# Kernel optimization log

Hardware: AMD Instinct MI355X
Metric: run time of the kernel (lower is better)

## Reference

```python
import jax, jax.numpy as jnp
import numpy as np
import math


def _strided_value_mask(L, S, dtype):
    # mask_line[L + d] == 0 when |d| is a power-of-two stride in {2,4,...,<=L};
    # value_mask[i, j] = mask_line[L - i + j], i.e. zero where |j - i| is such a stride.
    diff = jnp.abs(jnp.arange(L)[:, None] - jnp.arange(S)[None, :])  # [L, S]
    vm = jnp.ones((L, S), dtype=dtype)
    stride = 2
    while stride <= L:
        vm = vm * (diff != stride).astype(dtype)
        stride *= 2
    return vm


def setup_inputs() -> dict:
    key = jax.random.key(0)
    k1, k2, k3 = jax.random.split(key, 3)
    B, L, H, E = 4, 2048, 8, 64
    D = 64
    return {
        "queries": jax.random.normal(k1, (B, L, H, E), dtype=jnp.float32),
        "keys": jax.random.normal(k2, (B, L, H, E), dtype=jnp.float32),
        "values": jax.random.normal(k3, (B, L, H, D), dtype=jnp.float32),
    }


def reference(queries, keys, values):
    B, L, H, E = queries.shape
    S = keys.shape[1]
    scale = 1.0 / math.sqrt(E)

    # raw scores [B, H, L, S]
    scores = jnp.einsum("blhe,bshe->bhls", queries, keys)
    # multiplicative strided mask (zeroes scores at power-of-two offsets)
    vm = _strided_value_mask(L, S, scores.dtype)  # [L, S]
    scores = scores * vm
    # causal mask: upper triangle -> -inf (mask_flag=True, attn_mask=None path)
    causal = jnp.triu(jnp.ones((L, S), dtype=bool), k=1)
    scores = jnp.where(causal, -jnp.inf, scores)

    # dropout p=0.0 (eval) -> identity
    A = jax.nn.softmax(scale * scores, axis=-1)
    V = jnp.einsum("bhls,bshd->blhd", A, values)
    return V
```

## Files before the change

kernel.cpp:

```cpp
#include <hip/hip_runtime.h>
#include <hip/hip_bf16.h>
#include <stdint.h>

typedef __attribute__((ext_vector_type(8))) short short8;
typedef __attribute__((ext_vector_type(16))) float f32x16;

namespace {
constexpr int NB = 4, NL = 2048, NH = 8, NE = 64, ND = 64;
constexpr float KS = 0.125f * 1.44269504f;
constexpr int NCHUNK = 40;
constexpr int RECSZ  = 8320;
constexpr int KSTEP  = 64 * NH * NE;
}

__device__ const unsigned char TG[40] = {
  3,7,7,10,11,11,11,14,14,15,15,15,15,
  6,6,9,9,10,10,12,12,13,13,13,13,14,14,
  2,5,5,8,8,8,9,12,12,
  4,4,1,0};
__device__ const unsigned char TT0[40] = {
  0,0,16,0,0,16,32,0,16,0,16,32,48,
  0,14,0,14,16,30,0,14,0,14,28,42,32,46,
  0,0,12,0,12,24,28,28,40,
  0,10,0,0};
__device__ const unsigned char TT1[40] = {
  16,16,32,16,16,32,48,16,32,16,32,48,64,
  14,28,14,28,30,44,14,28,14,28,42,56,46,60,
  12,12,24,12,24,36,40,40,52,
  10,20,8,4};
__device__ const unsigned char TREC[40] = {
  3,10,11,18,21,22,23,32,33,36,37,38,39,
  8,9,15,16,19,20,24,25,28,29,30,31,34,35,
  2,6,7,12,13,14,17,26,27,
  4,5,1,0};
__device__ const unsigned char CUMD[16] = {0,1,2,3,4,6,8,10,12,15,18,21,24,28,32,36};
__device__ const unsigned char NCHD[16] = {1,1,1,1,2,2,2,2,3,3,3,3,4,4,4,4};

__device__ __forceinline__ ushort bfb(float x) {
  __hip_bfloat16 b(x);
  return __builtin_bit_cast(ushort, b);
}
__device__ __forceinline__ uint32_t pkbf(float lo, float hi) {
  return (uint32_t)bfb(lo) | ((uint32_t)bfb(hi) << 16);
}
__device__ __forceinline__ void glds16(const void* g, void* l) {
  __builtin_amdgcn_global_load_lds(
      (const __attribute__((address_space(1))) void*)g,
      (__attribute__((address_space(3))) void*)l, 16, 0, 0);
}

#define COMPUTE(TT, SUB, KB, VB) do {                                       \
    const int kv0_ = (TT) * 32;                                             \
    f32x16 s;                                                               \
    _Pragma("unroll")                                                       \
    for (int i_ = 0; i_ < 16; ++i_) s[i_] = 0.f;                            \
    { const char* kb_ = (const char*)(KB) + ((SUB)*32 + ln31) * 128;        \
      _Pragma("unroll")                                                     \
      for (int st_ = 0; st_ < 4; ++st_) {                                   \
        short8 kf_ = *(const short8*)(kb_ + ((st_*32 + hi*16) ^ rsw));      \
        s = __builtin_amdgcn_mfma_f32_32x32x16_bf16(kf_, qf[st_], s, 0,0,0);\
      } }                                                                   \
    const int delta_ = q0w - kv0_;                                          \
    const int qrelh_ = (qi - kv0_) - 4 * hi;                                \
    if ((TT) == tw) {                          \
      _Pragma("unroll")                                                     \
      for (int r_ = 0; r_ < 16; ++r_) {                                     \
        const int cr_ = (r_ & 3) + 8 * (r_ >> 2);                           \
        int diff_ = qrelh_ - cr_;                                           \
        float lg_ = s[r_];                                                  \
        bool p2_ = (diff_ > 1) & ((diff_ & (diff_ - 1)) == 0);              \
        lg_ = p2_ ? 0.f : lg_;                                              \
        lg_ = (diff_ < 0) ? -__builtin_inff() : lg_;                        \
        s[r_] = exp2f(lg_);                                                 \
      }                                                                     \
    } else {                                                                \
      int pmax_ = 1 << (31 - __clz(delta_ + 31));                           \
      if (pmax_ >= delta_ - 31) {        \
        _Pragma("unroll")                                                   \
        for (int r_ = 0; r_ < 16; ++r_) {                                   \
          const int cr_ = (r_ & 3) + 8 * (r_ >> 2);                         \
          int diff_ = qrelh_ - cr_;                                         \
          bool p2_ = (diff_ > 1) & ((diff_ & (diff_ - 1)) == 0);            \
          s[r_] = exp2f(p2_ ? 0.f : s[r_]);                                 \
        }                                                                   \
      } else {                                        \
        _Pragma("unroll")                                                   \
        for (int r_ = 0; r_ < 16; ++r_) s[r_] = exp2f(s[r_]);               \
      }                                                                     \
    }                                                                       \
    uint32_t w0_ = pkbf(s[0],  s[1]),  w1_ = pkbf(s[2],  s[3]);             \
    uint32_t w2_ = pkbf(s[4],  s[5]),  w3_ = pkbf(s[6],  s[7]);             \
    uint32_t w4_ = pkbf(s[8],  s[9]),  w5_ = pkbf(s[10], s[11]);            \
    uint32_t w6_ = pkbf(s[12], s[13]), w7_ = pkbf(s[14], s[15]);            \
    uint32_t y0_ = __shfl_xor(hi ? w0_ : w2_, 32);                          \
    uint32_t y1_ = __shfl_xor(hi ? w1_ : w3_, 32);                          \
    uint32_t y2_ = __shfl_xor(hi ? w4_ : w6_, 32);                          \
    uint32_t y3_ = __shfl_xor(hi ? w5_ : w7_, 32);                          \
    union { short8 v; uint32_t u[4]; } f0_, f1_;                            \
    if (hi == 0) {                                                          \
      f0_.u[0] = w0_; f0_.u[1] = w1_; f0_.u[2] = y0_; f0_.u[3] = y1_;       \
      f1_.u[0] = w4_; f1_.u[1] = w5_; f1_.u[2] = y2_; f1_.u[3] = y3_;       \
    } else {                                                                \
      f0_.u[0] = y0_; f0_.u[1] = y1_; f0_.u[2] = w2_; f0_.u[3] = w3_;       \
      f1_.u[0] = y2_; f1_.u[1] = y3_; f1_.u[2] = w6_; f1_.u[3] = w7_;       \
    }                                                                       \
    { const char* vr0_ = (const char*)(VB) + ln31 * 128;                    \
      const char* vr1_ = (const char*)(VB) + (32 + ln31) * 128;             \
      short8 a00_ = *(const short8*)(vr0_ + (((SUB)*64      + hi*16) ^ rsw));\
      short8 a01_ = *(const short8*)(vr0_ + (((SUB)*64 + 32 + hi*16) ^ rsw));\
      short8 a10_ = *(const short8*)(vr1_ + (((SUB)*64      + hi*16) ^ rsw));\
      short8 a11_ = *(const short8*)(vr1_ + (((SUB)*64 + 32 + hi*16) ^ rsw));\
      acc0 = __builtin_amdgcn_mfma_f32_32x32x16_bf16(a00_, f0_.v, acc0, 0,0,0); \
      acc0 = __builtin_amdgcn_mfma_f32_32x32x16_bf16(a01_, f1_.v, acc0, 0,0,0); \
      acc1 = __builtin_amdgcn_mfma_f32_32x32x16_bf16(a10_, f0_.v, acc1, 0,0,0); \
      acc1 = __builtin_amdgcn_mfma_f32_32x32x16_bf16(a11_, f1_.v, acc1, 0,0,0); \
      accl = __builtin_amdgcn_mfma_f32_32x32x16_bf16(onesv, f0_.v, accl, 0,0,0);\
      accl = __builtin_amdgcn_mfma_f32_32x32x16_bf16(onesv, f1_.v, accl, 0,0,0);\
    }                                                                       \
  } while (0)

#define LD(RR) do {                                                         \
    const float* kp_ = kpp + (size_t)(RR) * KSTEP;                          \
    const float* vp_ = vpp + (size_t)(RR) * KSTEP;                          \
    kx0 = *(const float4*)(kp_);      kx1 = *(const float4*)(kp_ + 4);      \
    kx2 = *(const float4*)(kp_ + 8);  kx3 = *(const float4*)(kp_ + 12);     \
    vx0 = *(const float4*)(vp_);               vx1 = *(const float4*)(vp_ + NH*ND); \
    vx2 = *(const float4*)(vp_ + 2*NH*ND);     vx3 = *(const float4*)(vp_ + 3*NH*ND); \
  } while (0)

#define STG(KB, VB) do {                                                    \
    uint4 kwA = { pkbf(kx0.x,kx0.y), pkbf(kx0.z,kx0.w),                     \
                  pkbf(kx1.x,kx1.y), pkbf(kx1.z,kx1.w) };                   \
    uint4 kwB = { pkbf(kx2.x,kx2.y), pkbf(kx2.z,kx2.w),                     \
                  pkbf(kx3.x,kx3.y), pkbf(kx3.z,kx3.w) };                   \
    *(uint4*)((KB) + krow*128 + ( kcol2        ^ kswz)) = kwA;              \
    *(uint4*)((KB) + krow*128 + ((kcol2 + 16)  ^ kswz)) = kwB;              \
    _Pragma("unroll")                                                       \
    for (int j_ = 0; j_ < 4; ++j_) {                                        \
      int d_ = vd0 + j_;                                                    \
      char* vr_ = (VB) + d_*128;                                            \
      int vs_ = (d_ & 7) << 4;                                              \
      *(uint32_t*)(vr_ + ((vk0*2    ) ^ vs_)) = pkbf(vx0[j_], vx1[j_]);     \
      *(uint32_t*)(vr_ + ((vk0*2 + 4) ^ vs_)) = pkbf(vx2[j_], vx3[j_]);     \
    }                                                                       \
  } while (0)

__global__ __launch_bounds__(256)
void convkv(const float* __restrict__ Kg, const float* __restrict__ Vg,
            char* __restrict__ kimg, char* __restrict__ vimg)
{
  const int id = blockIdx.x;
  const int kr = id & 31, bh = id >> 5;
  const int b = bh >> 3, h = bh & 7;
  const int tid = threadIdx.x;

  __shared__ float vt[64 * 64];

  const int key_in = tid >> 2;
  const int e0     = (tid & 3) * 16;
  {
    const float* vp = Vg + (((size_t)b * NL + kr * 64 + key_in) * NH + h) * ND + e0;
    float* dst = vt + key_in * 64 + e0;
    *(float4*)(dst)      = *(const float4*)(vp);
    *(float4*)(dst + 4)  = *(const float4*)(vp + 4);
    *(float4*)(dst + 8)  = *(const float4*)(vp + 8);
    *(float4*)(dst + 12) = *(const float4*)(vp + 12);
  }
  {
    const float* kp = Kg + (((size_t)b * NL + kr * 64 + key_in) * NH + h) * NE + e0;
    float4 a = *(const float4*)kp,     c = *(const float4*)(kp + 4);
    float4 d2 = *(const float4*)(kp + 8), f = *(const float4*)(kp + 12);
    uint4 wA = { pkbf(a.x,a.y), pkbf(a.z,a.w), pkbf(c.x,c.y), pkbf(c.z,c.w) };
    uint4 wB = { pkbf(d2.x,d2.y), pkbf(d2.z,d2.w), pkbf(f.x,f.y), pkbf(f.z,f.w) };
    char* ko = kimg + ((size_t)bh * 32 + kr) * 8192 + key_in * 128;
    const int C = (key_in & 7) << 4;
    *(uint4*)(ko + ((2 * e0)      ^ C)) = wA;
    *(uint4*)(ko + ((2 * e0 + 16) ^ C)) = wB;
  }
  __syncthreads();
  char* vo0 = vimg + ((size_t)bh * 32 + kr) * 8192;
  #pragma unroll
  for (int it = 0; it < 2; ++it) {
    int lin = it * 256 + tid;
    int d = lin & 63, kg = lin >> 6;
    const float* col = vt + kg * 8 * 64 + d;
    uint4 w = { pkbf(col[0], col[64]),   pkbf(col[128], col[192]),
                pkbf(col[256], col[320]), pkbf(col[384], col[448]) };
    *(uint4*)(vo0 + d * 128 + ((kg * 16) ^ ((d & 7) << 4))) = w;
  }
}

__global__ __launch_bounds__(256, 4)
void sattn_dma(const float* __restrict__ Qg, const char* __restrict__ kimg,
               const char* __restrict__ vimg, float* __restrict__ W)
{
  const int id = blockIdx.x;
  const int bh = id & 31;
  const int e  = id >> 5;
  const int g  = TG[e];
  const int t0 = TT0[e], t1 = TT1[e];
  float* rec = W + (size_t)(bh * NCHUNK + TREC[e]) * RECSZ;
  const int b = bh >> 3, h = bh & 7;

  const int tid  = threadIdx.x;
  const int wave = tid >> 6;
  const int lane = tid & 63;
  const int ln31 = lane & 31;
  const int hi   = lane >> 5;

  __shared__ __align__(16) char smem[2 * 16384];

  const int q0w = g * 128 + wave * 32;
  const int qi  = q0w + ln31;
  const int tw  = 4 * g + wave;
  const int rsw = (ln31 & 7) << 4;

  const char* kb_img = kimg + ((size_t)bh * 32 + (t0 >> 1)) * 8192;
  const char* vb_img = vimg + ((size_t)bh * 32 + (t0 >> 1)) * 8192;

#define STAGE(RR, PP) do {                                                  \
    const char* gb_ = (wave < 2 ? kb_img : vb_img)                          \
                      + (size_t)(RR) * 8192 + (wave & 1) * 4096;            \
    char* lb_ = smem + (PP) * 16384 + (wave < 2 ? 0 : 8192)                 \
                + (wave & 1) * 4096;                                        \
    _Pragma("unroll")                                                       \
    for (int c_ = 0; c_ < 4; ++c_)                                          \
      glds16(gb_ + c_ * 1024 + lane * 16, lb_ + c_ * 1024);                 \
  } while (0)

  short8 qf[4];
  {
    const float* qp = Qg + (((size_t)b * NL + qi) * NH + h) * NE;
    #pragma unroll
    for (int st = 0; st < 4; ++st) {
      const float* qpe = qp + st * 16 + hi * 8;
      union { short8 v; uint32_t u[4]; } f;
      #pragma unroll
      for (int j = 0; j < 4; ++j)
        f.u[j] = pkbf(qpe[2 * j] * KS, qpe[2 * j + 1] * KS);
      qf[st] = f.v;
    }
  }
  short8 onesv;
  {
    union { short8 v; uint32_t u[4]; } o;
    #pragma unroll
    for (int j = 0; j < 4; ++j) o.u[j] = 0x3F803F80u;
    onesv = o.v;
  }

  f32x16 acc0, acc1, accl;
  #pragma unroll
  for (int i = 0; i < 16; ++i) { acc0[i] = 0.f; acc1[i] = 0.f; accl[i] = 0.f; }

  const int nr = (t1 - t0) >> 1;
  STAGE(0, 0);
  __syncthreads();
  if (nr > 1) STAGE(1, 1);
  int p = 0;
  for (int r = 0; r < nr; ++r) {
    const int tt = t0 + 2 * r;
    const char* kc = smem + p * 16384;
    const char* vc = kc + 8192;
    if (tt     <= tw) COMPUTE(tt,     0, kc, vc);
    if (tt + 1 <= tw) COMPUTE(tt + 1, 1, kc, vc);
    if (r + 1 < nr) {
      __syncthreads();
      if (r + 2 < nr) STAGE(r + 2, p);
      p ^= 1;
    }
  }
#undef STAGE

  #pragma unroll
  for (int r = 0; r < 16; ++r) {
    int d = (r & 3) + 8 * (r >> 2) + 4 * hi;
    rec[d * 128 + wave * 32 + ln31]        = acc0[r];
    rec[(32 + d) * 128 + wave * 32 + ln31] = acc1[r];
  }
  if (hi == 0) rec[8192 + wave * 32 + ln31] = accl[0];
}

__global__ __launch_bounds__(256, 3)
void sattn_mid(const float* __restrict__ Qg, const float* __restrict__ Kg,
               const float* __restrict__ Vg, float* __restrict__ W)
{
  const int id = blockIdx.x;
  const int bh = id & 31;
  const int e  = id >> 5;
  const int g  = TG[e];
  const int t0 = TT0[e], t1 = TT1[e];
  float* rec = W + (size_t)(bh * NCHUNK + TREC[e]) * RECSZ;
  const int b = bh >> 3, h = bh & 7;

  const int tid  = threadIdx.x;
  const int wave = tid >> 6;
  const int lane = tid & 63;
  const int ln31 = lane & 31;
  const int hi   = lane >> 5;

  __shared__ __align__(16) struct { ushort kt[64 * 64]; ushort vt[64 * 64]; } lds;

  const int q0w = g * 128 + wave * 32;
  const int qi  = q0w + ln31;
  const int tw  = 4 * g + wave;
  const int rsw = (ln31 & 7) << 4;

  short8 qf[4];
  {
    const float* qp = Qg + (((size_t)b * NL + qi) * NH + h) * NE;
    #pragma unroll
    for (int st = 0; st < 4; ++st) {
      const float* qpe = qp + st * 16 + hi * 8;
      union { short8 v; uint32_t u[4]; } f;
      #pragma unroll
      for (int j = 0; j < 4; ++j)
        f.u[j] = pkbf(qpe[2 * j] * KS, qpe[2 * j + 1] * KS);
      qf[st] = f.v;
    }
  }
  short8 onesv;
  {
    union { short8 v; uint32_t u[4]; } o;
    #pragma unroll
    for (int j = 0; j < 4; ++j) o.u[j] = 0x3F803F80u;
    onesv = o.v;
  }

  f32x16 acc0, acc1, accl;
  #pragma unroll
  for (int i = 0; i < 16; ++i) { acc0[i] = 0.f; acc1[i] = 0.f; accl[i] = 0.f; }

  const int krow = tid >> 2,        kcol = (tid & 3) * 16;
  const int vk0  = (tid & 15) * 4,  vd0  = (tid >> 4) * 4;
  const int kbase = t0 * 32;
  const float* kpp = Kg + (((size_t)b * NL + kbase + krow) * NH + h) * NE + kcol;
  const float* vpp = Vg + (((size_t)b * NL + kbase + vk0 ) * NH + h) * ND + vd0;
  const int kswz  = (krow & 7) << 4;
  const int kcol2 = kcol * 2;

  float4 kx0, kx1, kx2, kx3, vx0, vx1, vx2, vx3;

  const int nr = (t1 - t0) >> 1;
  LD(0);
  STG((char*)lds.kt, (char*)lds.vt);
  __syncthreads();
  if (nr > 1) LD(1);
  for (int r = 0;;) {
    const int tt = t0 + 2 * r;
    if (tt     <= tw) COMPUTE(tt,     0, (char*)lds.kt, (char*)lds.vt);
    if (tt + 1 <= tw) COMPUTE(tt + 1, 1, (char*)lds.kt, (char*)lds.vt);
    if (++r == nr) break;
    __syncthreads();
    STG((char*)lds.kt, (char*)lds.vt);
    __syncthreads();
    if (r + 1 < nr) LD(r + 1);
  }

  #pragma unroll
  for (int r = 0; r < 16; ++r) {
    int d = (r & 3) + 8 * (r >> 2) + 4 * hi;
    rec[d * 128 + wave * 32 + ln31]        = acc0[r];
    rec[(32 + d) * 128 + wave * 32 + ln31] = acc1[r];
  }
  if (hi == 0) rec[8192 + wave * 32 + ln31] = accl[0];
}

__global__ __launch_bounds__(256)
void sattn_combine(const float* __restrict__ W, float* __restrict__ Og)
{
  const int id = blockIdx.x;
  const int h2 = id & 1, g = (id >> 1) & 15, bh = id >> 5;
  const int b = bh >> 3, h = bh & 7;
  const int tid = threadIdx.x;

  __shared__ float sd[64][67];
  __shared__ float Lq[64];

  const float* rec0 = W + (size_t)(bh * NCHUNK + CUMD[g]) * RECSZ;
  const int nc = NCHD[g];

  #pragma unroll
  for (int rep = 0; rep < 4; ++rep) {
    int d  = rep * 16 + (tid >> 4);
    int q4 = (tid & 15) * 4;
    float4 a = {0.f, 0.f, 0.f, 0.f};
    for (int c = 0; c < nc; ++c) {
      float4 v = *(const float4*)(rec0 + (size_t)c * RECSZ + d * 128 + h2 * 64 + q4);
      a.x += v.x; a.y += v.y; a.z += v.z; a.w += v.w;
    }
    sd[d][q4 + 0] = a.x; sd[d][q4 + 1] = a.y;
    sd[d][q4 + 2] = a.z; sd[d][q4 + 3] = a.w;
  }
  if (tid < 64) {
    float a = 0.f;
    for (int c = 0; c < nc; ++c) a += rec0[(size_t)c * RECSZ + 8192 + h2 * 64 + tid];
    Lq[tid] = 1.0f / a;
  }
  __syncthreads();
  #pragma unroll
  for (int rep = 0; rep < 4; ++rep) {
    int q  = rep * 16 + (tid >> 4);
    int d4 = (tid & 15) * 4;
    float l = Lq[q];
    float4 o = { sd[d4][q] * l, sd[d4 + 1][q] * l, sd[d4 + 2][q] * l, sd[d4 + 3][q] * l };
    *(float4*)(Og + (((size_t)b * NL + g * 128 + h2 * 64 + q) * NH + h) * ND + d4) = o;
  }
}

extern "C" void kernel_launch(void* const* d_in, const int* in_sizes, int n_in,
                              void* d_out, int out_size, void* d_ws, size_t ws_size,
                              hipStream_t stream) {
  const float* Q = (const float*)d_in[0];
  const float* K = (const float*)d_in[1];
  const float* V = (const float*)d_in[2];
  float* O = (float*)d_out;
  const size_t need_mid  = (size_t)32 * NCHUNK * RECSZ * sizeof(float);
  const size_t imgsz     = (size_t)32 * 32 * 8192;
  const size_t need_full = need_mid + 2 * imgsz;
  float* W = (float*)d_ws;
  if (ws_size >= need_full) {
    char* kimg = (char*)d_ws + need_mid;
    char* vimg = kimg + imgsz;
    convkv    <<<dim3(1024),        dim3(256), 0, stream>>>(K, V, kimg, vimg);
    sattn_dma <<<dim3(32 * NCHUNK), dim3(256), 0, stream>>>(Q, kimg, vimg, W);
    sattn_combine<<<dim3(1024),     dim3(256), 0, stream>>>(W, O);
  } else {
    sattn_mid <<<dim3(32 * NCHUNK), dim3(256), 0, stream>>>(Q, K, V, W);
    sattn_combine<<<dim3(1024),     dim3(256), 0, stream>>>(W, O);
  }
}
```

Before: 68.34 us.

## Replace block-shared LDS pipeline with independent per-wave work units reading bf16 images

The block-level attention kernel, which staged K/V tiles into LDS with double buffering and barriers, is replaced by a kernel where each wave owns a 32-query, up-to-16-tile work unit and reads the pre-converted bf16 K/V images straight from global memory. The row sum moves from an extra MFMA against a ones vector to a scalar accumulation. A new combine kernel reduces the finer 32-query partial records. This removes barriers and balances causal work at wave granularity, but gives up LDS reuse across waves, so every wave fetches its own K/V from global or cache, and the combine kernel has more records to sum.

```diff
diff --git a/kernel.cpp b/kernel.cpp
--- a/kernel.cpp
+++ b/kernel.cpp
@@ -8,6 +8,8 @@
 namespace {
 constexpr int NB = 4, NL = 2048, NH = 8, NE = 64, ND = 64;
 constexpr float KS = 0.125f * 1.44269504f;
+constexpr int RECSZ32 = 2080;
+constexpr int NUNIT   = 160;
 constexpr int NCHUNK = 40;
 constexpr int RECSZ  = 8320;
 constexpr int KSTEP  = 64 * NH * NE;
@@ -43,11 +45,264 @@
 __device__ __forceinline__ uint32_t pkbf(float lo, float hi) {
   return (uint32_t)bfb(lo) | ((uint32_t)bfb(hi) << 16);
 }
-__device__ __forceinline__ void glds16(const void* g, void* l) {
-  __builtin_amdgcn_global_load_lds(
-      (const __attribute__((address_space(1))) void*)g,
-      (__attribute__((address_space(3))) void*)l, 16, 0, 0);
-}
+
+
+__global__ __launch_bounds__(256)
+void convkv(const float* __restrict__ Kg, const float* __restrict__ Vg,
+            char* __restrict__ kimg, char* __restrict__ vimg)
+{
+  const int id = blockIdx.x;
+  const int kr = id & 31, bh = id >> 5;
+  const int b = bh >> 3, h = bh & 7;
+  const int tid = threadIdx.x;
+
+  __shared__ float vt[64 * 64];
+
+  const int key_in = tid >> 2;
+  const int e0     = (tid & 3) * 16;
+  {
+    const float* vp = Vg + (((size_t)b * NL + kr * 64 + key_in) * NH + h) * ND + e0;
+    float* dst = vt + key_in * 64 + e0;
+    *(float4*)(dst)      = *(const float4*)(vp);
+    *(float4*)(dst + 4)  = *(const float4*)(vp + 4);
+    *(float4*)(dst + 8)  = *(const float4*)(vp + 8);
+    *(float4*)(dst + 12) = *(const float4*)(vp + 12);
+  }
+  {
+    const float* kp = Kg + (((size_t)b * NL + kr * 64 + key_in) * NH + h) * NE + e0;
+    float4 a = *(const float4*)kp,      c = *(const float4*)(kp + 4);
+    float4 d2 = *(const float4*)(kp + 8), f = *(const float4*)(kp + 12);
+    uint4 wA = { pkbf(a.x,a.y), pkbf(a.z,a.w), pkbf(c.x,c.y), pkbf(c.z,c.w) };
+    uint4 wB = { pkbf(d2.x,d2.y), pkbf(d2.z,d2.w), pkbf(f.x,f.y), pkbf(f.z,f.w) };
+    char* ko = kimg + ((size_t)bh * 32 + kr) * 8192 + key_in * 128;
+    const int C = (key_in & 7) << 4;
+    *(uint4*)(ko + ((2 * e0)      ^ C)) = wA;
+    *(uint4*)(ko + ((2 * e0 + 16) ^ C)) = wB;
+  }
+  __syncthreads();
+  char* vo0 = vimg + ((size_t)bh * 32 + kr) * 8192;
+  #pragma unroll
+  for (int it = 0; it < 2; ++it) {
+    int lin = it * 256 + tid;
+    int d = lin & 63, kg = lin >> 6;
+    const float* col = vt + kg * 8 * 64 + d;
+    uint4 w = { pkbf(col[0], col[64]),    pkbf(col[128], col[192]),
+                pkbf(col[256], col[320]), pkbf(col[384], col[448]) };
+    *(uint4*)(vo0 + d * 128 + ((kg * 16) ^ ((d & 7) << 4))) = w;
+  }
+}
+
+__global__ __launch_bounds__(256)
+void sattn_wave(const float* __restrict__ Qg, const char* __restrict__ kimg,
+                const char* __restrict__ vimg, float* __restrict__ W)
+{
+  const int id   = blockIdx.x;
+  const int bh   = id & 31;
+  const int ublk = id >> 5;
+  const int b = bh >> 3, h = bh & 7;
+
+  const int tid  = threadIdx.x;
+  const int wave = tid >> 6;
+  const int lane = tid & 63;
+  const int ln31 = lane & 31;
+  const int hi   = lane >> 5;
+
+  const int u = ublk * 4 + wave;
+  int G, s, k;
+  if      (u < 16)  { G = 0; s = u;                 k = 0; }
+  else if (u < 48)  { G = 1; s = 16 + (u - 16) / 2; k = (u - 16) % 2; }
+  else if (u < 96)  { G = 2; s = 32 + (u - 48) / 3; k = (u - 48) % 3; }
+  else              { G = 3; s = 48 + (u - 96) / 4; k = (u - 96) % 4; }
+  (void)G;
+  const int t0u = 16 * k;
+  const int n   = s + 1;
+  const int t1u = (16 * (k + 1) < n) ? 16 * (k + 1) : n;
+
+  float* rec = W + ((size_t)bh * NUNIT + u) * RECSZ32;
+
+  const int q0w = s * 32;
+  const int qi  = q0w + ln31;
+  const int rsw = (ln31 & 7) << 4;
+  const char* kb_img = kimg + (size_t)bh * 32 * 8192;
+  const char* vb_img = vimg + (size_t)bh * 32 * 8192;
+
+  short8 qf[4];
+  {
+    const float* qp = Qg + (((size_t)b * NL + qi) * NH + h) * NE;
+    #pragma unroll
+    for (int st = 0; st < 4; ++st) {
+      const float* qpe = qp + st * 16 + hi * 8;
+      union { short8 v; uint32_t u[4]; } f;
+      #pragma unroll
+      for (int j = 0; j < 4; ++j)
+        f.u[j] = pkbf(qpe[2 * j] * KS, qpe[2 * j + 1] * KS);
+      qf[st] = f.v;
+    }
+  }
+
+  f32x16 acc0, acc1;
+  #pragma unroll
+  for (int i = 0; i < 16; ++i) { acc0[i] = 0.f; acc1[i] = 0.f; }
+  float ls = 0.f;
+
+  for (int t = t0u; t < t1u; ++t) {
+    const int kv0 = t * 32;
+    const char* kbase = kb_img + (size_t)(t >> 1) * 8192 + ((t & 1) * 32 + ln31) * 128;
+    const char* vbase = vb_img + (size_t)(t >> 1) * 8192;
+    const int   vsub  = (t & 1) * 64;
+
+    short8 a00 = *(const short8*)(vbase + ln31 * 128        + ((vsub      + hi * 16) ^ rsw));
+    short8 a01 = *(const short8*)(vbase + ln31 * 128        + ((vsub + 32 + hi * 16) ^ rsw));
+    short8 a10 = *(const short8*)(vbase + (32 + ln31) * 128 + ((vsub      + hi * 16) ^ rsw));
+    short8 a11 = *(const short8*)(vbase + (32 + ln31) * 128 + ((vsub + 32 + hi * 16) ^ rsw));
+
+    f32x16 sv;
+    #pragma unroll
+    for (int i = 0; i < 16; ++i) sv[i] = 0.f;
+    #pragma unroll
+    for (int st = 0; st < 4; ++st) {
+      short8 kf = *(const short8*)(kbase + ((st * 32 + hi * 16) ^ rsw));
+      sv = __builtin_amdgcn_mfma_f32_32x32x16_bf16(kf, qf[st], sv, 0, 0, 0);
+    }
+
+    const int delta = q0w - kv0;
+    const int qrelh = (qi - kv0) - 4 * hi;
+    float ps0 = 0.f, ps1 = 0.f;
+    if (t == s) {
+      #pragma unroll
+      for (int r = 0; r < 16; ++r) {
+        const int cr = (r & 3) + 8 * (r >> 2);
+        int diff = qrelh - cr;
+        float lg = sv[r];
+        bool p2 = (diff > 1) & ((diff & (diff - 1)) == 0);
+        lg = p2 ? 0.f : lg;
+        lg = (diff < 0) ? -__builtin_inff() : lg;
+        float p = exp2f(lg);
+        sv[r] = p; (r & 1 ? ps1 : ps0) += p;
+      }
+    } else {
+      int pmax = 1 << (31 - __clz(delta + 31));
+      if (pmax >= delta - 31) {
+        #pragma unroll
+        for (int r = 0; r < 16; ++r) {
+          const int cr = (r & 3) + 8 * (r >> 2);
+          int diff = qrelh - cr;
+          bool p2 = (diff > 1) & ((diff & (diff - 1)) == 0);
+          float p = exp2f(p2 ? 0.f : sv[r]);
+          sv[r] = p; (r & 1 ? ps1 : ps0) += p;
+        }
+      } else {
+        #pragma unroll
+        for (int r = 0; r < 16; ++r) {
+          float p = exp2f(sv[r]);
+          sv[r] = p; (r & 1 ? ps1 : ps0) += p;
+        }
+      }
+    }
+    ls += ps0 + ps1;
+
+    uint32_t w0 = pkbf(sv[0],  sv[1]),  w1 = pkbf(sv[2],  sv[3]);
+    uint32_t w2 = pkbf(sv[4],  sv[5]),  w3 = pkbf(sv[6],  sv[7]);
+    uint32_t w4 = pkbf(sv[8],  sv[9]),  w5 = pkbf(sv[10], sv[11]);
+    uint32_t w6 = pkbf(sv[12], sv[13]), w7 = pkbf(sv[14], sv[15]);
+    uint32_t y0 = __shfl_xor(hi ? w0 : w2, 32);
+    uint32_t y1 = __shfl_xor(hi ? w1 : w3, 32);
+    uint32_t y2 = __shfl_xor(hi ? w4 : w6, 32);
+    uint32_t y3 = __shfl_xor(hi ? w5 : w7, 32);
+    union { short8 v; uint32_t u[4]; } f0, f1;
+    if (hi == 0) {
+      f0.u[0] = w0; f0.u[1] = w1; f0.u[2] = y0; f0.u[3] = y1;
+      f1.u[0] = w4; f1.u[1] = w5; f1.u[2] = y2; f1.u[3] = y3;
+    } else {
+      f0.u[0] = y0; f0.u[1] = y1; f0.u[2] = w2; f0.u[3] = w3;
+      f1.u[0] = y2; f1.u[1] = y3; f1.u[2] = w6; f1.u[3] = w7;
+    }
+
+    acc0 = __builtin_amdgcn_mfma_f32_32x32x16_bf16(a00, f0.v, acc0, 0, 0, 0);
+    acc0 = __builtin_amdgcn_mfma_f32_32x32x16_bf16(a01, f1.v, acc0, 0, 0, 0);
+    acc1 = __builtin_amdgcn_mfma_f32_32x32x16_bf16(a10, f0.v, acc1, 0, 0, 0);
+    acc1 = __builtin_amdgcn_mfma_f32_32x32x16_bf16(a11, f1.v, acc1, 0, 0, 0);
+  }
+
+  ls += __shfl_xor(ls, 32);
+  #pragma unroll
+  for (int r = 0; r < 16; ++r) {
+    int d = (r & 3) + 8 * (r >> 2) + 4 * hi;
+    rec[d * 32 + ln31]        = acc0[r];
+    rec[(32 + d) * 32 + ln31] = acc1[r];
+  }
+  if (hi == 0) rec[2048 + ln31] = ls;
+}
+
+__global__ __launch_bounds__(256)
+void sattn_combine32(const float* __restrict__ W, float* __restrict__ Og)
+{
+  const int id = blockIdx.x;
+  const int s  = id & 63, bh = id >> 6;
+  const int b = bh >> 3, h = bh & 7;
+  const int tid = threadIdx.x;
+
+  const int G = s >> 4, i = s & 15;
+  const int cum = 8 * G * (G + 1) + i * (G + 1);
+  const int nc  = G + 1;
+  const float* rec0 = W + ((size_t)bh * NUNIT + cum) * RECSZ32;
+
+  __shared__ float sd[64][33];
+  __shared__ float Lq[32];
+
+  {
+    int d = tid >> 2, q4 = (tid & 3) * 8;
+    float4 a0 = {0,0,0,0}, a1 = {0,0,0,0};
+    for (int c = 0; c < nc; ++c) {
+      const float* rp = rec0 + (size_t)c * RECSZ32 + d * 32 + q4;
+      float4 v0 = *(const float4*)rp, v1 = *(const float4*)(rp + 4);
+      a0.x += v0.x; a0.y += v0.y; a0.z += v0.z; a0.w += v0.w;
+      a1.x += v1.x; a1.y += v1.y; a1.z += v1.z; a1.w += v1.w;
+    }
+    sd[d][q4+0] = a0.x; sd[d][q4+1] = a0.y; sd[d][q4+2] = a0.z; sd[d][q4+3] = a0.w;
+    sd[d][q4+4] = a1.x; sd[d][q4+5] = a1.y; sd[d][q4+6] = a1.z; sd[d][q4+7] = a1.w;
+  }
+  if (tid < 32) {
+    float a = 0.f;
+    for (int c = 0; c < nc; ++c) a += rec0[(size_t)c * RECSZ32 + 2048 + tid];
+    Lq[tid] = 1.0f / a;
+  }
+  __syncthreads();
+  {
+    int q = tid >> 3, d8 = (tid & 7) * 8;
+    float l = Lq[q];
+    float4 o0 = { sd[d8+0][q]*l, sd[d8+1][q]*l, sd[d8+2][q]*l, sd[d8+3][q]*l };
+    float4 o1 = { sd[d8+4][q]*l, sd[d8+5][q]*l, sd[d8+6][q]*l, sd[d8+7][q]*l };
+    float* op = Og + (((size_t)b * NL + s * 32 + q) * NH + h) * ND + d8;
+    *(float4*)op = o0; *(float4*)(op + 4) = o1;
+  }
+}
+
+#define LD(RR) do {                                                         \
+    const float* kp_ = kpp + (size_t)(RR) * KSTEP;                          \
+    const float* vp_ = vpp + (size_t)(RR) * KSTEP;                          \
+    kx0 = *(const float4*)(kp_);      kx1 = *(const float4*)(kp_ + 4);      \
+    kx2 = *(const float4*)(kp_ + 8);  kx3 = *(const float4*)(kp_ + 12);     \
+    vx0 = *(const float4*)(vp_);               vx1 = *(const float4*)(vp_ + NH*ND); \
+    vx2 = *(const float4*)(vp_ + 2*NH*ND);     vx3 = *(const float4*)(vp_ + 3*NH*ND); \
+  } while (0)
+
+#define STG(KB, VB) do {                                                    \
+    uint4 kwA = { pkbf(kx0.x,kx0.y), pkbf(kx0.z,kx0.w),                     \
+                  pkbf(kx1.x,kx1.y), pkbf(kx1.z,kx1.w) };                   \
+    uint4 kwB = { pkbf(kx2.x,kx2.y), pkbf(kx2.z,kx2.w),                     \
+                  pkbf(kx3.x,kx3.y), pkbf(kx3.z,kx3.w) };                   \
+    *(uint4*)((KB) + krow*128 + ( kcol2        ^ kswz)) = kwA;              \
+    *(uint4*)((KB) + krow*128 + ((kcol2 + 16)  ^ kswz)) = kwB;              \
+    _Pragma("unroll")                                                       \
+    for (int j_ = 0; j_ < 4; ++j_) {                                        \
+      int d_ = vd0 + j_;                                                    \
+      char* vr_ = (VB) + d_*128;                                            \
+      int vs_ = (d_ & 7) << 4;                                              \
+      *(uint32_t*)(vr_ + ((vk0*2    ) ^ vs_)) = pkbf(vx0[j_], vx1[j_]);     \
+      *(uint32_t*)(vr_ + ((vk0*2 + 4) ^ vs_)) = pkbf(vx2[j_], vx3[j_]);     \
+    }                                                                       \
+  } while (0)
 
 #define COMPUTE(TT, SUB, KB, VB) do {                                       \
     const int kv0_ = (TT) * 32;                                             \
@@ -62,7 +317,7 @@
       } }                                                                   \
     const int delta_ = q0w - kv0_;                                          \
     const int qrelh_ = (qi - kv0_) - 4 * hi;                                \
-    if ((TT) == tw) {                          \
+    if ((TT) == tw) {                                                       \
       _Pragma("unroll")                                                     \
       for (int r_ = 0; r_ < 16; ++r_) {                                     \
         const int cr_ = (r_ & 3) + 8 * (r_ >> 2);                           \
@@ -75,7 +330,7 @@
       }                                                                     \
     } else {                                                                \
       int pmax_ = 1 << (31 - __clz(delta_ + 31));                           \
-      if (pmax_ >= delta_ - 31) {        \
+      if (pmax_ >= delta_ - 31) {                                           \
         _Pragma("unroll")                                                   \
         for (int r_ = 0; r_ < 16; ++r_) {                                   \
           const int cr_ = (r_ & 3) + 8 * (r_ >> 2);                         \
@@ -83,7 +338,7 @@
           bool p2_ = (diff_ > 1) & ((diff_ & (diff_ - 1)) == 0);            \
           s[r_] = exp2f(p2_ ? 0.f : s[r_]);                                 \
         }                                                                   \
-      } else {                                        \
+      } else {                                                              \
         _Pragma("unroll")                                                   \
         for (int r_ = 0; r_ < 16; ++r_) s[r_] = exp2f(s[r_]);               \
       }                                                                     \
@@ -119,168 +374,6 @@
     }                                                                       \
   } while (0)
 
-#define LD(RR) do {                                                         \
-    const float* kp_ = kpp + (size_t)(RR) * KSTEP;                          \
-    const float* vp_ = vpp + (size_t)(RR) * KSTEP;                          \
-    kx0 = *(const float4*)(kp_);      kx1 = *(const float4*)(kp_ + 4);      \
-    kx2 = *(const float4*)(kp_ + 8);  kx3 = *(const float4*)(kp_ + 12);     \
-    vx0 = *(const float4*)(vp_);               vx1 = *(const float4*)(vp_ + NH*ND); \
-    vx2 = *(const float4*)(vp_ + 2*NH*ND);     vx3 = *(const float4*)(vp_ + 3*NH*ND); \
-  } while (0)
-
-#define STG(KB, VB) do {                                                    \
-    uint4 kwA = { pkbf(kx0.x,kx0.y), pkbf(kx0.z,kx0.w),                     \
-                  pkbf(kx1.x,kx1.y), pkbf(kx1.z,kx1.w) };                   \
-    uint4 kwB = { pkbf(kx2.x,kx2.y), pkbf(kx2.z,kx2.w),                     \
-                  pkbf(kx3.x,kx3.y), pkbf(kx3.z,kx3.w) };                   \
-    *(uint4*)((KB) + krow*128 + ( kcol2        ^ kswz)) = kwA;              \
-    *(uint4*)((KB) + krow*128 + ((kcol2 + 16)  ^ kswz)) = kwB;              \
-    _Pragma("unroll")                                                       \
-    for (int j_ = 0; j_ < 4; ++j_) {                                        \
-      int d_ = vd0 + j_;                                                    \
-      char* vr_ = (VB) + d_*128;                                            \
-      int vs_ = (d_ & 7) << 4;                                              \
-      *(uint32_t*)(vr_ + ((vk0*2    ) ^ vs_)) = pkbf(vx0[j_], vx1[j_]);     \
-      *(uint32_t*)(vr_ + ((vk0*2 + 4) ^ vs_)) = pkbf(vx2[j_], vx3[j_]);     \
-    }                                                                       \
-  } while (0)
-
-__global__ __launch_bounds__(256)
-void convkv(const float* __restrict__ Kg, const float* __restrict__ Vg,
-            char* __restrict__ kimg, char* __restrict__ vimg)
-{
-  const int id = blockIdx.x;
-  const int kr = id & 31, bh = id >> 5;
-  const int b = bh >> 3, h = bh & 7;
-  const int tid = threadIdx.x;
-
-  __shared__ float vt[64 * 64];
-
-  const int key_in = tid >> 2;
-  const int e0     = (tid & 3) * 16;
-  {
-    const float* vp = Vg + (((size_t)b * NL + kr * 64 + key_in) * NH + h) * ND + e0;
-    float* dst = vt + key_in * 64 + e0;
-    *(float4*)(dst)      = *(const float4*)(vp);
-    *(float4*)(dst + 4)  = *(const float4*)(vp + 4);
-    *(float4*)(dst + 8)  = *(const float4*)(vp + 8);
-    *(float4*)(dst + 12) = *(const float4*)(vp + 12);
-  }
-  {
-    const float* kp = Kg + (((size_t)b * NL + kr * 64 + key_in) * NH + h) * NE + e0;
-    float4 a = *(const float4*)kp,     c = *(const float4*)(kp + 4);
-    float4 d2 = *(const float4*)(kp + 8), f = *(const float4*)(kp + 12);
-    uint4 wA = { pkbf(a.x,a.y), pkbf(a.z,a.w), pkbf(c.x,c.y), pkbf(c.z,c.w) };
-    uint4 wB = { pkbf(d2.x,d2.y), pkbf(d2.z,d2.w), pkbf(f.x,f.y), pkbf(f.z,f.w) };
-    char* ko = kimg + ((size_t)bh * 32 + kr) * 8192 + key_in * 128;
-    const int C = (key_in & 7) << 4;
-    *(uint4*)(ko + ((2 * e0)      ^ C)) = wA;
-    *(uint4*)(ko + ((2 * e0 + 16) ^ C)) = wB;
-  }
-  __syncthreads();
-  char* vo0 = vimg + ((size_t)bh * 32 + kr) * 8192;
-  #pragma unroll
-  for (int it = 0; it < 2; ++it) {
-    int lin = it * 256 + tid;
-    int d = lin & 63, kg = lin >> 6;
-    const float* col = vt + kg * 8 * 64 + d;
-    uint4 w = { pkbf(col[0], col[64]),   pkbf(col[128], col[192]),
-                pkbf(col[256], col[320]), pkbf(col[384], col[448]) };
-    *(uint4*)(vo0 + d * 128 + ((kg * 16) ^ ((d & 7) << 4))) = w;
-  }
-}
-
-__global__ __launch_bounds__(256, 4)
-void sattn_dma(const float* __restrict__ Qg, const char* __restrict__ kimg,
-               const char* __restrict__ vimg, float* __restrict__ W)
-{
-  const int id = blockIdx.x;
-  const int bh = id & 31;
-  const int e  = id >> 5;
-  const int g  = TG[e];
-  const int t0 = TT0[e], t1 = TT1[e];
-  float* rec = W + (size_t)(bh * NCHUNK + TREC[e]) * RECSZ;
-  const int b = bh >> 3, h = bh & 7;
-
-  const int tid  = threadIdx.x;
-  const int wave = tid >> 6;
-  const int lane = tid & 63;
-  const int ln31 = lane & 31;
-  const int hi   = lane >> 5;
-
-  __shared__ __align__(16) char smem[2 * 16384];
-
-  const int q0w = g * 128 + wave * 32;
-  const int qi  = q0w + ln31;
-  const int tw  = 4 * g + wave;
-  const int rsw = (ln31 & 7) << 4;
-
-  const char* kb_img = kimg + ((size_t)bh * 32 + (t0 >> 1)) * 8192;
-  const char* vb_img = vimg + ((size_t)bh * 32 + (t0 >> 1)) * 8192;
-
-#define STAGE(RR, PP) do {                                                  \
-    const char* gb_ = (wave < 2 ? kb_img : vb_img)                          \
-                      + (size_t)(RR) * 8192 + (wave & 1) * 4096;            \
-    char* lb_ = smem + (PP) * 16384 + (wave < 2 ? 0 : 8192)                 \
-                + (wave & 1) * 4096;                                        \
-    _Pragma("unroll")                                                       \
-    for (int c_ = 0; c_ < 4; ++c_)                                          \
-      glds16(gb_ + c_ * 1024 + lane * 16, lb_ + c_ * 1024);                 \
-  } while (0)
-
-  short8 qf[4];
-  {
-    const float* qp = Qg + (((size_t)b * NL + qi) * NH + h) * NE;
-    #pragma unroll
-    for (int st = 0; st < 4; ++st) {
-      const float* qpe = qp + st * 16 + hi * 8;
-      union { short8 v; uint32_t u[4]; } f;
-      #pragma unroll
-      for (int j = 0; j < 4; ++j)
-        f.u[j] = pkbf(qpe[2 * j] * KS, qpe[2 * j + 1] * KS);
-      qf[st] = f.v;
-    }
-  }
-  short8 onesv;
-  {
-    union { short8 v; uint32_t u[4]; } o;
-    #pragma unroll
-    for (int j = 0; j < 4; ++j) o.u[j] = 0x3F803F80u;
-    onesv = o.v;
-  }
-
-  f32x16 acc0, acc1, accl;
-  #pragma unroll
-  for (int i = 0; i < 16; ++i) { acc0[i] = 0.f; acc1[i] = 0.f; accl[i] = 0.f; }
-
-  const int nr = (t1 - t0) >> 1;
-  STAGE(0, 0);
-  __syncthreads();
-  if (nr > 1) STAGE(1, 1);
-  int p = 0;
-  for (int r = 0; r < nr; ++r) {
-    const int tt = t0 + 2 * r;
-    const char* kc = smem + p * 16384;
-    const char* vc = kc + 8192;
-    if (tt     <= tw) COMPUTE(tt,     0, kc, vc);
-    if (tt + 1 <= tw) COMPUTE(tt + 1, 1, kc, vc);
-    if (r + 1 < nr) {
-      __syncthreads();
-      if (r + 2 < nr) STAGE(r + 2, p);
-      p ^= 1;
-    }
-  }
-#undef STAGE
-
-  #pragma unroll
-  for (int r = 0; r < 16; ++r) {
-    int d = (r & 3) + 8 * (r >> 2) + 4 * hi;
-    rec[d * 128 + wave * 32 + ln31]        = acc0[r];
-    rec[(32 + d) * 128 + wave * 32 + ln31] = acc1[r];
-  }
-  if (hi == 0) rec[8192 + wave * 32 + ln31] = accl[0];
-}
-
 __global__ __launch_bounds__(256, 3)
 void sattn_mid(const float* __restrict__ Qg, const float* __restrict__ Kg,
                const float* __restrict__ Vg, float* __restrict__ W)
@@ -415,18 +508,19 @@
   const float* K = (const float*)d_in[1];
   const float* V = (const float*)d_in[2];
   float* O = (float*)d_out;
+  const size_t recbytes = (size_t)32 * NUNIT * RECSZ32 * sizeof(float);
+  const size_t imgsz    = (size_t)32 * 32 * 8192;
+  const size_t need_full = recbytes + 2 * imgsz;
   const size_t need_mid  = (size_t)32 * NCHUNK * RECSZ * sizeof(float);
-  const size_t imgsz     = (size_t)32 * 32 * 8192;
-  const size_t need_full = need_mid + 2 * imgsz;
   float* W = (float*)d_ws;
   if (ws_size >= need_full) {
-    char* kimg = (char*)d_ws + need_mid;
+    char* kimg = (char*)d_ws + recbytes;
     char* vimg = kimg + imgsz;
-    convkv    <<<dim3(1024),        dim3(256), 0, stream>>>(K, V, kimg, vimg);
-    sattn_dma <<<dim3(32 * NCHUNK), dim3(256), 0, stream>>>(Q, kimg, vimg, W);
-    sattn_combine<<<dim3(1024),     dim3(256), 0, stream>>>(W, O);
+    convkv        <<<dim3(1024), dim3(256), 0, stream>>>(K, V, kimg, vimg);
+    sattn_wave    <<<dim3(1280), dim3(256), 0, stream>>>(Q, kimg, vimg, W);
+    sattn_combine32<<<dim3(2048), dim3(256), 0, stream>>>(W, O);
   } else {
-    sattn_mid <<<dim3(32 * NCHUNK), dim3(256), 0, stream>>>(Q, K, V, W);
-    sattn_combine<<<dim3(1024),     dim3(256), 0, stream>>>(W, O);
-  }
-}
+    sattn_mid     <<<dim3(32 * NCHUNK), dim3(256), 0, stream>>>(Q, K, V, W);
+    sattn_combine <<<dim3(1024), dim3(256), 0, stream>>>(W, O);
+  }
+}
```

Measured after the change: 73.18 us. 7.1% more time.
